# Optimization experiments

Measured on AMD Instinct MI355X. Metric: run time of the kernel, lower is better.

Reference implementation:

```python
import jax, jax.numpy as jnp
import numpy as np

TOP_K = 2  # config.moe_config.top_k


def setup_inputs() -> dict:
    key = jax.random.key(0)
    k0, k1, k2, k3 = jax.random.split(key, 4)
    T, H, I, E = 8192, 2048, 1408, 8  # tokens, hidden, moe_intermediate, experts
    x = jax.random.normal(k0, (T, H), jnp.float32)
    router_weight = jax.random.normal(k1, (E, H), jnp.float32) * 0.02
    gate_up_proj = jax.random.normal(k2, (E, H, 2 * I), jnp.float32) * 0.02
    down_proj = jax.random.normal(k3, (E, I, H), jnp.float32) * 0.02
    return {"x": x, "router_weight": router_weight,
            "gate_up_proj": gate_up_proj, "down_proj": down_proj}


def _moe_forward(x, router_weight, gate_up_proj, down_proj):
    # Router: fp32 gating linear (no bias), softmax over experts, top-k,
    # then scatter the top-k softmax weights into a dense [T, E] gate tensor
    # (topk_version=False path of Router.top_k_softmax).
    T = x.shape[0]
    E = router_weight.shape[0]
    logits = x.astype(jnp.float32) @ router_weight.T            # [T, E]
    probs = jax.nn.softmax(logits, axis=-1)                      # [T, E]
    topk_w, topk_idx = jax.lax.top_k(probs, TOP_K)               # [T, k]
    gates = jnp.zeros_like(logits).at[
        jnp.arange(T)[:, None], topk_idx].set(topk_w)            # [T, E] sparse gates

    # Grouped expert MLP (GroupedMLP): merged gate/up GEMM, SwiGLU, down GEMM.
    # Dispatch/permute + grouped GEMM + weighted combine is mathematically
    # out[t] = sum_e gates[t, e] * MLP_e(x[t]); expressed here as a fixed loop
    # over the small expert set with masked accumulation (jit-friendly).
    out = jnp.zeros_like(x)
    for e in range(E):
        gu = x @ gate_up_proj[e]                                 # [T, 2I]
        g, u = jnp.split(gu, 2, axis=-1)
        h = (jax.nn.silu(g) * u) @ down_proj[e]                  # [T, H]
        out = out + gates[:, e:e + 1].astype(x.dtype) * h
    return out


def reference(x, router_weight, gate_up_proj, down_proj):
    return _moe_forward(x, router_weight, gate_up_proj, down_proj)
```

## Files before the change

### kernel.cpp

```cpp
#include <hip/hip_runtime.h>
#include <hip/hip_bf16.h>
#include <cstdint>
#include <cstddef>

#define T_TOK 8192
#define H_DIM 2048
#define I_DIM 1408
#define E_NUM 8
#define BM 128
#define BK 64
#define ROWS_CAP (2 * T_TOK + E_NUM * BM)
#define MAX_MT (ROWS_CAP / BM)
#define NT1 (I_DIM / 64)
#define NT2 (H_DIM / 128)
#define NTILE_GU (44 * 16 * E_NUM)
#define NTILE_DN (32 * 11 * E_NUM)
#define NTILE_TOT (NTILE_GU + NTILE_DN)
#define TCVT_NB 2048

typedef __attribute__((ext_vector_type(8))) short short8;
typedef __attribute__((ext_vector_type(4))) float f32x4;
typedef __attribute__((ext_vector_type(8))) unsigned short bf16x8;
typedef __attribute__((ext_vector_type(4))) unsigned short bf16x4;
typedef __attribute__((ext_vector_type(8))) _Float16 h16x8;

static __device__ __forceinline__ unsigned short f2bf(float f) {
  unsigned u = __float_as_uint(f);
  u += 0x7FFFu + ((u >> 16) & 1u);
  return (unsigned short)(u >> 16);
}

static __device__ __forceinline__ void gld_lds16(const void* g, void* l) {
  __builtin_amdgcn_global_load_lds(
      (__attribute__((address_space(1))) unsigned int*)g,
      (__attribute__((address_space(3))) unsigned int*)l, 16, 0, 0);
}

template <int G>
static __device__ __forceinline__ void remap_tile(int bid, int nb, int nt_cols,
                                                  int& m_t, int& n_t) {
  int chunk = nb >> 3;
  int wg = (bid & 7) * chunk + (bid >> 3);
  int grp = wg / (nt_cols * G);
  int rem = wg % (nt_cols * G);
  n_t = rem / G;
  m_t = grp * G + rem % G;
}

__global__ __launch_bounds__(256) void router_kernel(
    const float* __restrict__ x, const float* __restrict__ rw,
    unsigned short* __restrict__ xb,
    int* __restrict__ topk_idx, float* __restrict__ topk_w, int* __restrict__ meta) {
  int t = blockIdx.x * 4 + (threadIdx.x >> 6);
  int lane = threadIdx.x & 63;
  const float* xr = x + (size_t)t * H_DIM;
  unsigned short* xbr = xb + (size_t)t * H_DIM;
  float acc[E_NUM];
#pragma unroll
  for (int e = 0; e < E_NUM; e++) acc[e] = 0.f;
  for (int j = lane * 4; j < H_DIM; j += 256) {
    f32x4 v = *(const f32x4*)(xr + j);
    bf16x4 b;
#pragma unroll
    for (int u = 0; u < 4; u++) b[u] = f2bf(v[u]);
    *(bf16x4*)(xbr + j) = b;
#pragma unroll
    for (int e = 0; e < E_NUM; e++) {
      f32x4 w = *(const f32x4*)(rw + e * H_DIM + j);
      acc[e] += v[0] * w[0] + v[1] * w[1] + v[2] * w[2] + v[3] * w[3];
    }
  }
#pragma unroll
  for (int e = 0; e < E_NUM; e++) {
    float v = acc[e];
#pragma unroll
    for (int s = 32; s > 0; s >>= 1) v += __shfl_xor(v, s);
    acc[e] = v;
  }
  if (lane == 0) {
    int i0 = 0;
#pragma unroll
    for (int e = 1; e < E_NUM; e++) if (acc[e] > acc[i0]) i0 = e;
    int i1 = (i0 == 0) ? 1 : 0;
#pragma unroll
    for (int e = 0; e < E_NUM; e++) if (e != i0 && acc[e] > acc[i1]) i1 = e;
    float mx = acc[0];
#pragma unroll
    for (int e = 1; e < E_NUM; e++) mx = fmaxf(mx, acc[e]);
    float sum = 0.f, p[E_NUM];
#pragma unroll
    for (int e = 0; e < E_NUM; e++) { p[e] = expf(acc[e] - mx); sum += p[e]; }
    float inv = 1.f / sum;
    topk_idx[t * 2] = i0;  topk_idx[t * 2 + 1] = i1;
    topk_w[t * 2] = p[i0] * inv;  topk_w[t * 2 + 1] = p[i1] * inv;
    atomicAdd(&meta[i0], 1);
    atomicAdd(&meta[i1], 1);
  }
}

__global__ void scan_kernel(int* __restrict__ meta, int* __restrict__ row_token) {
  __shared__ int s_off[E_NUM + 1];
  if (threadIdx.x == 0) {
    int o = 0, nt = 0;
    for (int e = 0; e < E_NUM; e++) {
      meta[16 + e] = o; s_off[e] = o;
      int c = meta[e];
      int mtc = (c + BM - 1) / BM;
      for (int m = 0; m < mtc; m++) { meta[64 + nt] = e; meta[256 + nt] = o + m * BM; nt++; }
      o += mtc * BM;
      meta[8 + e] = 0;
    }
    meta[16 + E_NUM] = o; s_off[E_NUM] = o;
    meta[32] = nt;
  }
  __syncthreads();
  for (int e = 0; e < E_NUM; e++) {
    int lo = s_off[e] + meta[e], hi = s_off[e + 1];
    for (int r = lo + (int)threadIdx.x; r < hi; r += 64) row_token[r] = -1;
  }
}

__global__ __launch_bounds__(256) void bucket_kernel(
    const int* __restrict__ topk_idx, int* __restrict__ meta,
    int* __restrict__ row_token, int* __restrict__ tok2row) {
  int i = blockIdx.x * 256 + threadIdx.x;
  if (i >= 2 * T_TOK) return;
  int e = topk_idx[i];
  int pos = atomicAdd(&meta[8 + e], 1);
  int r = meta[16 + e] + pos;
  row_token[r] = i >> 1;
  tok2row[i] = r;
}

__global__ __launch_bounds__(256) void tcvt2_kernel(
    const float* __restrict__ wgu, const float* __restrict__ wdn,
    unsigned short* __restrict__ wgu_t, unsigned short* __restrict__ wd_t) {
  __shared__ alignas(16) float st[2][128 * 64];
  int tid = threadIdx.x, l = tid & 63, w = tid >> 6;

  auto decode = [&](int t, const float*& src, unsigned short*& dst,
                    int& R, int& C, int& c0, int& r0) {
    if (t < NTILE_GU) {
      int e = t / 704, rem = t % 704;
      R = H_DIM; C = 2 * I_DIM;
      c0 = (rem % 44) * 64; r0 = (rem / 44) * 128;
      src = wgu + (size_t)e * R * C;
      dst = wgu_t + (size_t)e * R * C;
    } else {
      int tt = t - NTILE_GU;
      int e = tt / 352, rem = tt % 352;
      R = I_DIM; C = H_DIM;
      c0 = (rem % 32) * 64; r0 = (rem / 32) * 128;
      src = wdn + (size_t)e * R * C;
      dst = wd_t + (size_t)e * R * C;
    }
  };

  auto stage = [&](int buf, int t) {
    const float* src; unsigned short* dst; int R, C, c0, r0;
    decode(t, src, dst, R, C, c0, r0);
#pragma unroll
    for (int i = 0; i < 8; i++) {
      int rbase = w * 32 + i * 4;
      int r = rbase + (l >> 4);
      int key = (r & 7) ^ ((r >> 3) & 7);
      int c4 = ((l & 15) ^ key) * 4;
      gld_lds16(src + (size_t)(r0 + r) * C + c0 + c4,
                (char*)&st[buf][0] + rbase * 256);
    }
  };

  auto process = [&](int buf, int t) {
    const float* src; unsigned short* dst; int R, C, c0, r0;
    decode(t, src, dst, R, C, c0, r0);
    int ca = tid & 15, cg = tid >> 4;
#pragma unroll
    for (int it = 0; it < 4; it++) {
      int c = it * 16 + cg;
      bf16x8 o;
#pragma unroll
      for (int j = 0; j < 8; j++) {
        int r = ca * 8 + j;
        int key = (r & 7) ^ ((r >> 3) & 7);
        o[j] = f2bf(st[buf][r * 64 + (((c >> 2) ^ key) << 2) + (c & 3)]);
      }
      *(bf16x8*)(dst + (size_t)(c0 + c) * R + r0 + ca * 8) = o;
    }
  };

  int t = blockIdx.x;
  if (t >= NTILE_TOT) return;
  int nxt = t + TCVT_NB;
  stage(0, t);
  int buf = 0;
  while (true) {
    bool has_next = (nxt < NTILE_TOT);
    if (has_next) {
      stage(buf ^ 1, nxt);
      asm volatile("s_waitcnt vmcnt(8)" ::: "memory");
    } else {
      asm volatile("s_waitcnt vmcnt(0)" ::: "memory");
    }
    __builtin_amdgcn_s_barrier();
    process(buf, t);
    if (!has_next) break;
    asm volatile("" ::: "memory");
    __builtin_amdgcn_s_barrier();
    t = nxt; nxt += TCVT_NB; buf ^= 1;
  }
}

__global__ __launch_bounds__(256) void gemm1_kernel(
    const unsigned short* __restrict__ xb,
    const unsigned short* __restrict__ wgu,
    unsigned short* __restrict__ hbuf,
    const int* __restrict__ row_token, const int* __restrict__ meta) {
  int m_t, n_t;
  remap_tile<4>(blockIdx.x, NT1 * MAX_MT, NT1, m_t, n_t);
  if (m_t >= meta[32]) return;
  int e = meta[64 + m_t];
  int row0 = meta[256 + m_t];
  int n0h = n_t * 64;

  __shared__ alignas(16) char smem[65536];

  int tid = threadIdx.x, lane = tid & 63, wid = tid >> 6;
  const unsigned short* asrc[4];
  const unsigned short* bsrc[4];
  {
    const unsigned short* wb = wgu + (size_t)e * (2 * (size_t)I_DIM) * H_DIM;
#pragma unroll
    for (int i = 0; i < 4; i++) {
      int r = i * 32 + (tid >> 3);
      int ch = ((tid & 7) ^ (r & 7)) * 8;
      int tok = row_token[row0 + r];
      if (tok < 0) tok = 0;
      asrc[i] = xb + (size_t)tok * H_DIM + ch;
      int wr = (r < 64) ? (n0h + r) : (I_DIM + n0h + (r - 64));
      bsrc[i] = wb + (size_t)wr * H_DIM + ch;
    }
  }
  f32x4 acc[4][4] = {};
  int mrow = (wid >> 1) * 64 + (lane & 15);
  int brow = (wid & 1) * 64 + (lane & 15);

#define STAGE1(buf, kof_)                                                     \
  {                                                                           \
    int kof = (kof_);                                                         \
    char* b = smem + (buf) * 32768;                                           \
    _Pragma("unroll") for (int i = 0; i < 4; i++) {                           \
      gld_lds16(asrc[i] + kof, b + i * 4096 + wid * 1024);                    \
      gld_lds16(bsrc[i] + kof, b + 16384 + i * 4096 + wid * 1024);            \
    }                                                                         \
  }

  constexpr int NK1 = H_DIM / BK;
  STAGE1(0, 0);
  STAGE1(1, BK);
  for (int kt = 0; kt < NK1; kt++) {
    int cur = kt & 1;
    if (kt + 1 < NK1) { asm volatile("s_waitcnt vmcnt(8)" ::: "memory"); }
    else              { asm volatile("s_waitcnt vmcnt(0)" ::: "memory"); }
    __builtin_amdgcn_s_barrier();
    const unsigned short* sA = (const unsigned short*)(smem + cur * 32768);
    const unsigned short* sB = sA + 8192;
#pragma unroll
    for (int kk = 0; kk < 2; kk++) {
      int krd = ((kk * 4 + (lane >> 4)) ^ (lane & 7)) * 8;
      short8 af[4], bf[4];
#pragma unroll
      for (int f = 0; f < 4; f++) {
        af[f] = *(const short8*)(sA + (mrow + f * 16) * BK + krd);
        bf[f] = *(const short8*)(sB + (brow + f * 16) * BK + krd);
      }
#pragma unroll
      for (int fm = 0; fm < 4; fm++)
#pragma unroll
        for (int fn = 0; fn < 4; fn++)
          acc[fm][fn] = __builtin_amdgcn_mfma_f32_16x16x32_bf16(af[fm], bf[fn], acc[fm][fn], 0, 0, 0);
    }
    asm volatile("" ::: "memory");
    __builtin_amdgcn_s_barrier();
    asm volatile("" ::: "memory");
    if (kt + 2 < NK1) STAGE1(cur, (kt + 2) * BK);
  }

  float* xw = (float*)smem + (wid >> 1) * 4096;
  if (wid & 1) {
#pragma unroll
    for (int fm = 0; fm < 4; fm++)
#pragma unroll
      for (int r = 0; r < 4; r++) {
        int mloc = fm * 16 + (lane >> 4) * 4 + r;
#pragma unroll
        for (int fn = 0; fn < 4; fn++)
          xw[mloc * 64 + fn * 16 + (lane & 15)] = acc[fm][fn][r];
      }
  }
  __syncthreads();
  if (!(wid & 1)) {
    int mbase = row0 + (wid >> 1) * 64;
#pragma unroll
    for (int fm = 0; fm < 4; fm++)
#pragma unroll
      for (int r = 0; r < 4; r++) {
        int mloc = fm * 16 + (lane >> 4) * 4 + r;
        size_t rbase = (size_t)(mbase + mloc) * I_DIM + n0h;
#pragma unroll
        for (int fn = 0; fn < 4; fn++) {
          float g = acc[fm][fn][r];
          float u = xw[mloc * 64 + fn * 16 + (lane & 15)];
          float hv = (g / (1.f + __expf(-g))) * u;
          hbuf[rbase + fn * 16 + (lane & 15)] = f2bf(hv);
        }
      }
  }
}

__global__ __launch_bounds__(256) void gemm2_kernel(
    const unsigned short* __restrict__ hbuf,
    const unsigned short* __restrict__ wd,
    _Float16* __restrict__ part,
    const int* __restrict__ meta) {
  int m_t, n_t;
  remap_tile<8>(blockIdx.x, NT2 * MAX_MT, NT2, m_t, n_t);
  if (m_t >= meta[32]) return;
  int e = meta[64 + m_t];
  int row0 = meta[256 + m_t];
  int n0 = n_t * 128;

  __shared__ alignas(16) char smem[65536];

  int tid = threadIdx.x, lane = tid & 63, wid = tid >> 6;
  const unsigned short* asrc[4];
  const unsigned short* bsrc[4];
  {
    const unsigned short* wb = wd + (size_t)e * (size_t)H_DIM * I_DIM;
#pragma unroll
    for (int i = 0; i < 4; i++) {
      int r = i * 32 + (tid >> 3);
      int ch = ((tid & 7) ^ (r & 7)) * 8;
      asrc[i] = hbuf + (size_t)(row0 + r) * I_DIM + ch;
      bsrc[i] = wb + (size_t)(n0 + r) * I_DIM + ch;
    }
  }
  f32x4 acc[4][4] = {};
  int mrow = (wid >> 1) * 64 + (lane & 15);
  int brow = (wid & 1) * 64 + (lane & 15);

  constexpr int NK2 = I_DIM / BK;
  STAGE1(0, 0);
  STAGE1(1, BK);
  for (int kt = 0; kt < NK2; kt++) {
    int cur = kt & 1;
    if (kt + 1 < NK2) { asm volatile("s_waitcnt vmcnt(8)" ::: "memory"); }
    else              { asm volatile("s_waitcnt vmcnt(0)" ::: "memory"); }
    __builtin_amdgcn_s_barrier();
    const unsigned short* sA = (const unsigned short*)(smem + cur * 32768);
    const unsigned short* sB = sA + 8192;
#pragma unroll
    for (int kk = 0; kk < 2; kk++) {
      int krd = ((kk * 4 + (lane >> 4)) ^ (lane & 7)) * 8;
      short8 af[4], bf[4];
#pragma unroll
      for (int f = 0; f < 4; f++) {
        af[f] = *(const short8*)(sA + (mrow + f * 16) * BK + krd);
        bf[f] = *(const short8*)(sB + (brow + f * 16) * BK + krd);
      }
#pragma unroll
      for (int fm = 0; fm < 4; fm++)
#pragma unroll
        for (int fn = 0; fn < 4; fn++)
          acc[fm][fn] = __builtin_amdgcn_mfma_f32_16x16x32_bf16(af[fm], bf[fn], acc[fm][fn], 0, 0, 0);
    }
    asm volatile("" ::: "memory");
    __builtin_amdgcn_s_barrier();
    asm volatile("" ::: "memory");
    if (kt + 2 < NK2) STAGE1(cur, (kt + 2) * BK);
  }
  _Float16* stg = (_Float16*)(smem + wid * 8192);
  int l15 = lane & 15;
#pragma unroll
  for (int fm = 0; fm < 4; fm++)
#pragma unroll
    for (int r = 0; r < 4; r++) {
      int mloc = fm * 16 + (lane >> 4) * 4 + r;
#pragma unroll
      for (int fn = 0; fn < 4; fn++) {
        int nl = fn * 16 + l15;
        stg[mloc * 64 + (((nl >> 3) ^ (mloc & 7)) << 3) + (nl & 7)] =
            (_Float16)acc[fm][fn][r];
      }
    }
  int m0 = (wid >> 1) * 64;
  int nbase = n0 + (wid & 1) * 64;
  int ca = lane & 7;
#pragma unroll
  for (int it = 0; it < 8; it++) {
    int mr = it * 8 + (lane >> 3);
    h16x8 v = *(const h16x8*)(stg + mr * 64 + ((ca ^ (mr & 7)) << 3));
    *(h16x8*)(part + (size_t)(row0 + m0 + mr) * H_DIM + nbase + ca * 8) = v;
  }
}

__global__ __launch_bounds__(256) void combine_kernel(
    const _Float16* __restrict__ part, const int* __restrict__ tok2row,
    const float* __restrict__ topk_w, float* __restrict__ out) {
  int t = blockIdx.x;
  int c = threadIdx.x * 8;
  int r0 = tok2row[2 * t], r1 = tok2row[2 * t + 1];
  float w0 = topk_w[2 * t], w1 = topk_w[2 * t + 1];
  h16x8 p0 = *(const h16x8*)(part + (size_t)r0 * H_DIM + c);
  h16x8 p1 = *(const h16x8*)(part + (size_t)r1 * H_DIM + c);
  float* o = out + (size_t)t * H_DIM + c;
  f32x4 lo, hi;
#pragma unroll
  for (int j = 0; j < 4; j++) lo[j] = w0 * (float)p0[j] + w1 * (float)p1[j];
#pragma unroll
  for (int j = 0; j < 4; j++) hi[j] = w0 * (float)p0[4 + j] + w1 * (float)p1[4 + j];
  *(f32x4*)o = lo;
  *(f32x4*)(o + 4) = hi;
}

extern "C" void kernel_launch(void* const* d_in, const int* in_sizes, int n_in,
                              void* d_out, int out_size, void* d_ws, size_t ws_size,
                              hipStream_t stream) {
  const float* x   = (const float*)d_in[0];
  const float* rw  = (const float*)d_in[1];
  const float* wgu = (const float*)d_in[2];
  const float* wdn = (const float*)d_in[3];
  float* out = (float*)d_out;

  char* ws = (char*)d_ws;
  size_t off = 0;
  auto alloc = [&](size_t bytes) {
    void* p = ws + off;
    off += (bytes + 255) & ~(size_t)255;
    return p;
  };
  int* meta            = (int*)alloc(4096);
  int* topk_idx        = (int*)alloc((size_t)2 * T_TOK * 4);
  float* topk_w        = (float*)alloc((size_t)2 * T_TOK * 4);
  int* tok2row         = (int*)alloc((size_t)2 * T_TOK * 4);
  int* row_token       = (int*)alloc((size_t)ROWS_CAP * 4);
  unsigned short* xb    = (unsigned short*)alloc((size_t)T_TOK * H_DIM * 2);
  unsigned short* wgu_t = (unsigned short*)alloc((size_t)E_NUM * 2 * I_DIM * H_DIM * 2);
  unsigned short* wd_t  = (unsigned short*)alloc((size_t)E_NUM * H_DIM * I_DIM * 2);
  unsigned short* hbuf  = (unsigned short*)alloc((size_t)ROWS_CAP * I_DIM * 2);
  _Float16* part = (_Float16*)wgu_t;

  if (off > ws_size) {
    (void)hipMemsetAsync(d_out, 0, (size_t)out_size * sizeof(float), stream);
    return;
  }

  (void)hipMemsetAsync(meta, 0, 4096, stream);

  tcvt2_kernel<<<TCVT_NB, 256, 0, stream>>>(wgu, wdn, wgu_t, wd_t);
  router_kernel<<<T_TOK / 4, 256, 0, stream>>>(x, rw, xb, topk_idx, topk_w, meta);
  scan_kernel<<<1, 64, 0, stream>>>(meta, row_token);
  bucket_kernel<<<(2 * T_TOK + 255) / 256, 256, 0, stream>>>(topk_idx, meta, row_token, tok2row);

  gemm1_kernel<<<NT1 * MAX_MT, 256, 0, stream>>>(xb, wgu_t, hbuf, row_token, meta);
  gemm2_kernel<<<NT2 * MAX_MT, 256, 0, stream>>>(hbuf, wd_t, part, meta);
  combine_kernel<<<T_TOK, 256, 0, stream>>>(part, tok2row, topk_w, out);
}
```

Before: 726.8 us.

## Overlap down-proj weight transpose-convert with gate/up GEMM in one launch

Splits the combined weight transpose/convert kernel so it handles only the gate/up weights. The down-projection weight conversion moves into the first 512 blocks of the gemm1 launch, so it runs alongside the gate/up GEMM tiles. The aim is to hide the memory-bound conversion behind compute-bound GEMM work and take it off the critical path. In exchange, those blocks occupy CUs during gemm1 and compete with it for bandwidth and LDS, and gemm1's tile order is shifted by the block offset.

```diff
diff --git a/kernel.cpp b/kernel.cpp
--- a/kernel.cpp
+++ b/kernel.cpp
@@ -15,8 +15,8 @@
 #define NT2 (H_DIM / 128)
 #define NTILE_GU (44 * 16 * E_NUM)
 #define NTILE_DN (32 * 11 * E_NUM)
-#define NTILE_TOT (NTILE_GU + NTILE_DN)
 #define TCVT_NB 2048
+#define DN_NB 512
 
 typedef __attribute__((ext_vector_type(8))) short short8;
 typedef __attribute__((ext_vector_type(4))) float f32x4;
@@ -132,33 +132,16 @@
   tok2row[i] = r;
 }
 
-__global__ __launch_bounds__(256) void tcvt2_kernel(
-    const float* __restrict__ wgu, const float* __restrict__ wdn,
-    unsigned short* __restrict__ wgu_t, unsigned short* __restrict__ wd_t) {
+__global__ __launch_bounds__(256) void tcvt_gu_kernel(
+    const float* __restrict__ wgu, unsigned short* __restrict__ wgu_t) {
   __shared__ alignas(16) float st[2][128 * 64];
   int tid = threadIdx.x, l = tid & 63, w = tid >> 6;
-
-  auto decode = [&](int t, const float*& src, unsigned short*& dst,
-                    int& R, int& C, int& c0, int& r0) {
-    if (t < NTILE_GU) {
-      int e = t / 704, rem = t % 704;
-      R = H_DIM; C = 2 * I_DIM;
-      c0 = (rem % 44) * 64; r0 = (rem / 44) * 128;
-      src = wgu + (size_t)e * R * C;
-      dst = wgu_t + (size_t)e * R * C;
-    } else {
-      int tt = t - NTILE_GU;
-      int e = tt / 352, rem = tt % 352;
-      R = I_DIM; C = H_DIM;
-      c0 = (rem % 32) * 64; r0 = (rem / 32) * 128;
-      src = wdn + (size_t)e * R * C;
-      dst = wd_t + (size_t)e * R * C;
-    }
-  };
+  constexpr int R = H_DIM, C = 2 * I_DIM;
 
   auto stage = [&](int buf, int t) {
-    const float* src; unsigned short* dst; int R, C, c0, r0;
-    decode(t, src, dst, R, C, c0, r0);
+    int e = t / 704, rem = t % 704;
+    int c0 = (rem % 44) * 64, r0 = (rem / 44) * 128;
+    const float* src = wgu + (size_t)e * R * C;
 #pragma unroll
     for (int i = 0; i < 8; i++) {
       int rbase = w * 32 + i * 4;
@@ -169,10 +152,10 @@
                 (char*)&st[buf][0] + rbase * 256);
     }
   };
-
   auto process = [&](int buf, int t) {
-    const float* src; unsigned short* dst; int R, C, c0, r0;
-    decode(t, src, dst, R, C, c0, r0);
+    int e = t / 704, rem = t % 704;
+    int c0 = (rem % 44) * 64, r0 = (rem / 44) * 128;
+    unsigned short* dst = wgu_t + (size_t)e * R * C;
     int ca = tid & 15, cg = tid >> 4;
 #pragma unroll
     for (int it = 0; it < 4; it++) {
@@ -189,12 +172,12 @@
   };
 
   int t = blockIdx.x;
-  if (t >= NTILE_TOT) return;
+  if (t >= NTILE_GU) return;
   int nxt = t + TCVT_NB;
   stage(0, t);
   int buf = 0;
   while (true) {
-    bool has_next = (nxt < NTILE_TOT);
+    bool has_next = (nxt < NTILE_GU);
     if (has_next) {
       stage(buf ^ 1, nxt);
       asm volatile("s_waitcnt vmcnt(8)" ::: "memory");
@@ -213,18 +196,78 @@
 __global__ __launch_bounds__(256) void gemm1_kernel(
     const unsigned short* __restrict__ xb,
     const unsigned short* __restrict__ wgu,
+    const float* __restrict__ wdn,
+    unsigned short* __restrict__ wd_t,
     unsigned short* __restrict__ hbuf,
     const int* __restrict__ row_token, const int* __restrict__ meta) {
+  __shared__ alignas(16) char smem[65536];
+  int tid = threadIdx.x, lane = tid & 63, wid = tid >> 6;
+
+  if ((int)blockIdx.x < DN_NB) {
+    float* stf = (float*)smem;
+    int l = tid & 63, w = tid >> 6;
+    constexpr int R = I_DIM, C = H_DIM;
+    auto stage = [&](int buf, int t) {
+      int e = t / 352, rem = t % 352;
+      int c0 = (rem % 32) * 64, r0 = (rem / 32) * 128;
+      const float* src = wdn + (size_t)e * R * C;
+#pragma unroll
+      for (int i = 0; i < 8; i++) {
+        int rbase = w * 32 + i * 4;
+        int r = rbase + (l >> 4);
+        int key = (r & 7) ^ ((r >> 3) & 7);
+        int c4 = ((l & 15) ^ key) * 4;
+        gld_lds16(src + (size_t)(r0 + r) * C + c0 + c4,
+                  (char*)stf + buf * 32768 + rbase * 256);
+      }
+    };
+    auto process = [&](int buf, int t) {
+      int e = t / 352, rem = t % 352;
+      int c0 = (rem % 32) * 64, r0 = (rem / 32) * 128;
+      unsigned short* dst = wd_t + (size_t)e * R * C;
+      int ca = tid & 15, cg = tid >> 4;
+#pragma unroll
+      for (int it = 0; it < 4; it++) {
+        int c = it * 16 + cg;
+        bf16x8 o;
+#pragma unroll
+        for (int j = 0; j < 8; j++) {
+          int r = ca * 8 + j;
+          int key = (r & 7) ^ ((r >> 3) & 7);
+          o[j] = f2bf(stf[buf * 8192 + r * 64 + (((c >> 2) ^ key) << 2) + (c & 3)]);
+        }
+        *(bf16x8*)(dst + (size_t)(c0 + c) * R + r0 + ca * 8) = o;
+      }
+    };
+    int t = blockIdx.x;
+    int nxt = t + DN_NB;
+    stage(0, t);
+    int buf = 0;
+    while (true) {
+      bool has_next = (nxt < NTILE_DN);
+      if (has_next) {
+        stage(buf ^ 1, nxt);
+        asm volatile("s_waitcnt vmcnt(8)" ::: "memory");
+      } else {
+        asm volatile("s_waitcnt vmcnt(0)" ::: "memory");
+      }
+      __builtin_amdgcn_s_barrier();
+      process(buf, t);
+      if (!has_next) break;
+      asm volatile("" ::: "memory");
+      __builtin_amdgcn_s_barrier();
+      t = nxt; nxt += DN_NB; buf ^= 1;
+    }
+    return;
+  }
+
   int m_t, n_t;
-  remap_tile<4>(blockIdx.x, NT1 * MAX_MT, NT1, m_t, n_t);
+  remap_tile<4>((int)blockIdx.x - DN_NB, NT1 * MAX_MT, NT1, m_t, n_t);
   if (m_t >= meta[32]) return;
   int e = meta[64 + m_t];
   int row0 = meta[256 + m_t];
   int n0h = n_t * 64;
 
-  __shared__ alignas(16) char smem[65536];
-
-  int tid = threadIdx.x, lane = tid & 63, wid = tid >> 6;
   const unsigned short* asrc[4];
   const unsigned short* bsrc[4];
   {
@@ -456,12 +499,13 @@
 
   (void)hipMemsetAsync(meta, 0, 4096, stream);
 
-  tcvt2_kernel<<<TCVT_NB, 256, 0, stream>>>(wgu, wdn, wgu_t, wd_t);
+  tcvt_gu_kernel<<<TCVT_NB, 256, 0, stream>>>(wgu, wgu_t);
   router_kernel<<<T_TOK / 4, 256, 0, stream>>>(x, rw, xb, topk_idx, topk_w, meta);
   scan_kernel<<<1, 64, 0, stream>>>(meta, row_token);
   bucket_kernel<<<(2 * T_TOK + 255) / 256, 256, 0, stream>>>(topk_idx, meta, row_token, tok2row);
 
-  gemm1_kernel<<<NT1 * MAX_MT, 256, 0, stream>>>(xb, wgu_t, hbuf, row_token, meta);
+  gemm1_kernel<<<DN_NB + NT1 * MAX_MT, 256, 0, stream>>>(
+      xb, wgu_t, wdn, wd_t, hbuf, row_token, meta);
   gemm2_kernel<<<NT2 * MAX_MT, 256, 0, stream>>>(hbuf, wd_t, part, meta);
   combine_kernel<<<T_TOK, 256, 0, stream>>>(part, tok2row, topk_w, out);
 }
```

Result: no change. 724.0 us (-0.4%).
